# Optimization experiments

Measured on AMD Instinct MI355X. Metric: run time of the kernel, lower is better.

## Reference

```python
import jax, jax.numpy as jnp
import numpy as np
import math

HIDDEN = 2048
HEADS = 16
GROUPS = 4
HEAD_DIM = HIDDEN // HEADS  # 128
KV_DIM = GROUPS * HEAD_DIM  # 512
B, S = 2, 2048


def setup_inputs() -> dict:
    key = jax.random.key(0)
    ks = jax.random.split(key, 10)
    scale = 0.02
    return {
        "X": jax.random.normal(ks[0], (B, S, HIDDEN), dtype=jnp.float32),
        "attention_mask": jnp.ones((B, S), dtype=jnp.int32),
        "Wq": jax.random.normal(ks[1], (HIDDEN, HIDDEN), dtype=jnp.float32) * scale,
        "bq": jnp.zeros((HIDDEN,), dtype=jnp.float32),
        "Wk": jax.random.normal(ks[2], (HIDDEN, KV_DIM), dtype=jnp.float32) * scale,
        "bk": jnp.zeros((KV_DIM,), dtype=jnp.float32),
        "Wv": jax.random.normal(ks[3], (HIDDEN, KV_DIM), dtype=jnp.float32) * scale,
        "bv": jnp.zeros((KV_DIM,), dtype=jnp.float32),
        "Wo": jax.random.normal(ks[4], (HIDDEN, HIDDEN), dtype=jnp.float32) * scale,
        "bo": jnp.zeros((HIDDEN,), dtype=jnp.float32),
    }


def reference(X, attention_mask, Wq, bq, Wk, bk, Wv, bv, Wo, bo):
    b, s, _ = X.shape
    num_per_group = HEADS // GROUPS
    # projections
    Q = (X @ Wq + bq).reshape(b, s, HEADS, HEAD_DIM).transpose(0, 2, 1, 3)   # [b,H,s,d]
    K = (X @ Wk + bk).reshape(b, s, GROUPS, HEAD_DIM).transpose(0, 2, 1, 3)  # [b,G,s,d]
    V = (X @ Wv + bv).reshape(b, s, GROUPS, HEAD_DIM).transpose(0, 2, 1, 3)
    # torch .repeat(1, num_per_group, 1, 1) tiles group axis: [g0..gG-1, g0..gG-1, ...]
    K = jnp.tile(K, (1, num_per_group, 1, 1))  # [b,H,s,d]
    V = jnp.tile(V, (1, num_per_group, 1, 1))
    scores = jnp.einsum("bhqd,bhkd->bhqk", Q, K) / math.sqrt(HEAD_DIM)
    mask = attention_mask[:, None, None, :] == 0  # [b,1,1,s]
    scores = jnp.where(mask, jnp.float32(-jnp.inf), scores)
    attn = jax.nn.softmax(scores, axis=-1)
    out = jnp.einsum("bhqk,bhkd->bhqd", attn, V)  # [b,H,s,d]
    out = out.transpose(0, 2, 1, 3).reshape(b, s, HIDDEN)
    return out @ Wo + bo
```

## Files before the change

### kernel.cpp

```cpp
#include <hip/hip_runtime.h>
#include <hip/hip_bf16.h>


typedef __attribute__((ext_vector_type(8))) short short8;
typedef __attribute__((ext_vector_type(4))) short short4v;
typedef __attribute__((ext_vector_type(4))) float float4v;

#define C1F 0.12751743f
#define B0F -16.0f

#if defined(__has_builtin) && __has_builtin(__builtin_amdgcn_exp2f)
#define EXP2(x) __builtin_amdgcn_exp2f(x)
#else
#define EXP2(x) exp2f(x)
#endif

__device__ __forceinline__ short f2bf(float x) {
    __hip_bfloat16 h = __float2bfloat16(x);
    short s; __builtin_memcpy(&s, &h, sizeof(s)); return s;
}

__device__ __forceinline__ void gl16(const short* g, short* l) {
    __builtin_amdgcn_global_load_lds(
        (const __attribute__((address_space(1))) void*)g,
        (__attribute__((address_space(3))) void*)l, 16, 0, 0);
}

__global__ __launch_bounds__(256) void cvt_bf16_kernel(const float* __restrict__ in,
                                                       short* __restrict__ out, int n) {
    int i = (blockIdx.x * 256 + threadIdx.x) * 4;
    if (i >= n) return;
    float4 v = *(const float4*)(in + i);
    short4v o;
    o[0] = f2bf(v.x); o[1] = f2bf(v.y); o[2] = f2bf(v.z); o[3] = f2bf(v.w);
    *(short4v*)(out + i) = o;
}

__global__ __launch_bounds__(256) void transpose_cvt_kernel(const float* __restrict__ W,
                                                            short* __restrict__ Wt,
                                                            int K, int N) {
    __shared__ float tile[32][33];
    int n0 = blockIdx.x * 32, k0 = blockIdx.y * 32;
    int tx = threadIdx.x & 31, ty = threadIdx.x >> 5;
#pragma unroll
    for (int i = 0; i < 4; ++i) {
        int kk = ty + i * 8;
        tile[kk][tx] = W[(size_t)(k0 + kk) * N + n0 + tx];
    }
    __syncthreads();
#pragma unroll
    for (int i = 0; i < 4; ++i) {
        int nn = ty + i * 8;
        Wt[(size_t)(n0 + nn) * K + k0 + tx] = f2bf(tile[tx][nn]);
    }
}

__global__ __launch_bounds__(256) void gemm_dma_kernel(
    const short* __restrict__ A, const short* __restrict__ Bt,
    const float* __restrict__ b0, const float* __restrict__ b1, const float* __restrict__ b2,
    short* __restrict__ O0, short* __restrict__ O1, short* __restrict__ O2,
    float* __restrict__ Of, int K, int mode) {
    __shared__ short As[128 * 32];
    __shared__ short Bs[128 * 32];
    const int t = threadIdx.x, lane = t & 63, w = t >> 6;
    const int l15 = lane & 15, quad = lane >> 4;
    const int wm = (w & 1) * 64, wn = (w >> 1) * 64;
    const int m0 = blockIdx.y * 128, n0 = blockIdx.x * 128;
    const int r4 = lane >> 2, c8 = (lane & 3) * 8;
    const short* ga = A + (size_t)(m0 + w * 16 + r4) * K + c8;
    const short* gb = Bt + (size_t)(n0 + w * 16 + r4) * K + c8;
    short* lA = As + (w * 16) * 32;
    short* lB = Bs + (w * 16) * 32;

    float4v acc[4][4] = {};

    for (int k0 = 0; k0 < K; k0 += 32) {
        gl16(ga + k0, lA);
        gl16(ga + (size_t)64 * K + k0, lA + 64 * 32);
        gl16(gb + k0, lB);
        gl16(gb + (size_t)64 * K + k0, lB + 64 * 32);
        __syncthreads();
        short8 af[4], bfr[4];
#pragma unroll
        for (int i = 0; i < 4; ++i)
            af[i] = *(const short8*)(As + (wm + i * 16 + l15) * 32 + quad * 8);
#pragma unroll
        for (int j = 0; j < 4; ++j)
            bfr[j] = *(const short8*)(Bs + (wn + j * 16 + l15) * 32 + quad * 8);
#pragma unroll
        for (int i = 0; i < 4; ++i)
#pragma unroll
            for (int j = 0; j < 4; ++j)
                acc[i][j] = __builtin_amdgcn_mfma_f32_16x16x32_bf16(af[i], bfr[j], acc[i][j], 0, 0, 0);
        __syncthreads();
    }

#pragma unroll
    for (int i = 0; i < 4; ++i) {
#pragma unroll
        for (int j = 0; j < 4; ++j) {
            const int col = n0 + wn + j * 16 + l15;
            const int row0 = m0 + wm + i * 16 + quad * 4;
            if (mode == 1) {
                const float bc = b0[col];
#pragma unroll
                for (int r = 0; r < 4; ++r)
                    Of[(size_t)(row0 + r) * 2048 + col] = acc[i][j][r] + bc;
            } else if (col < 2048) {
                const float bc = b0[col];
#pragma unroll
                for (int r = 0; r < 4; ++r)
                    O0[(size_t)(row0 + r) * 2048 + col] = f2bf(acc[i][j][r] + bc);
            } else if (col < 2560) {
                const int c = col - 2048;
                const float bc = b1[c];
#pragma unroll
                for (int r = 0; r < 4; ++r)
                    O1[(size_t)(row0 + r) * 512 + c] = f2bf(acc[i][j][r] + bc);
            } else {
                const int c = col - 2560;
                const float bc = b2[c];
#pragma unroll
                for (int r = 0; r < 4; ++r)
                    O2[(size_t)c * 4096 + row0 + r] = f2bf(acc[i][j][r] + bc);
            }
        }
    }
}

__global__ __launch_bounds__(512, 2) void flash_kernel(
    const short* __restrict__ Qb, const short* __restrict__ Kb,
    const short* __restrict__ Vt, const int* __restrict__ mask,
    short* __restrict__ Ab) {
    __shared__ short Ks[64 * 136];
    __shared__ short Vs[128 * 72];
    __shared__ short Ps[8 * 32 * 72];
    __shared__ float mb[64];

    const int t = threadIdx.x;
    const int lane = t & 63, w = t >> 6;
    const int l15 = lane & 15, quad = lane >> 4;
    const int qt = blockIdx.x, g = blockIdx.y, b = blockIdx.z;
    const int h = g + 4 * (w & 3);
    const int q0 = qt * 64 + (w >> 2) * 32;

    short8 qf[2][4];
#pragma unroll
    for (int mi = 0; mi < 2; ++mi)
#pragma unroll
        for (int ks = 0; ks < 4; ++ks)
            qf[mi][ks] = *(const short8*)(Qb + (size_t)(b * 2048 + q0 + mi * 16 + l15) * 2048
                                          + h * 128 + ks * 32 + quad * 8);

    float4v o[2][8] = {};
    float rsum[2][4] = {};
    short* PsW = Ps + w * (32 * 72);

    const int kR = t >> 4, kC = (t & 15) * 8;
    const int vR = t >> 3, vC = (t & 7) * 8;
    const short* kg = Kb + (size_t)(b * 2048 + kR) * 512 + g * 128 + kC;
    const short* vg = Vt + (size_t)(g * 128 + vR) * 4096 + (size_t)b * 2048 + vC;

    for (int kt = 0; kt < 32; ++kt) {
        const int kb = kt * 64;
        short8 k0v = *(const short8*)(kg + (size_t)kb * 512);
        short8 k1v = *(const short8*)(kg + (size_t)(kb + 32) * 512);
        short8 v0v = *(const short8*)(vg + kb);
        short8 v1v = *(const short8*)(vg + (size_t)64 * 4096 + kb);
        float mv = 0.f;
        if (t < 64) mv = mask[b * 2048 + kb + t] ? B0F : -1e30f;
        __syncthreads();
        *(short8*)(Ks + kR * 136 + kC) = k0v;
        *(short8*)(Ks + (kR + 32) * 136 + kC) = k1v;
        *(short8*)(Vs + vR * 72 + vC) = v0v;
        *(short8*)(Vs + (vR + 64) * 72 + vC) = v1v;
        if (t < 64) mb[t] = mv;
        __syncthreads();

        float4v s[2][4] = {};
#pragma unroll
        for (int ks = 0; ks < 4; ++ks)
#pragma unroll
            for (int j = 0; j < 4; ++j) {
                short8 bk = *(const short8*)(Ks + (j * 16 + l15) * 136 + ks * 32 + quad * 8);
                s[0][j] = __builtin_amdgcn_mfma_f32_16x16x32_bf16(qf[0][ks], bk, s[0][j], 0, 0, 0);
                s[1][j] = __builtin_amdgcn_mfma_f32_16x16x32_bf16(qf[1][ks], bk, s[1][j], 0, 0, 0);
            }
#pragma unroll
        for (int mi = 0; mi < 2; ++mi)
#pragma unroll
            for (int j = 0; j < 4; ++j) {
                const float mbias = mb[j * 16 + l15];
#pragma unroll
                for (int r = 0; r < 4; ++r) {
                    float p = EXP2(fmaf(s[mi][j][r], C1F, mbias));
                    rsum[mi][r] += p;
                    PsW[(mi * 16 + quad * 4 + r) * 72 + j * 16 + l15] = f2bf(p);
                }
            }
#pragma unroll
        for (int ks2 = 0; ks2 < 2; ++ks2) {
            short8 pa0 = *(const short8*)(PsW + l15 * 72 + ks2 * 32 + quad * 8);
            short8 pa1 = *(const short8*)(PsW + (16 + l15) * 72 + ks2 * 32 + quad * 8);
#pragma unroll
            for (int jj = 0; jj < 8; ++jj) {
                short8 bv = *(const short8*)(Vs + (jj * 16 + l15) * 72 + ks2 * 32 + quad * 8);
                o[0][jj] = __builtin_amdgcn_mfma_f32_16x16x32_bf16(pa0, bv, o[0][jj], 0, 0, 0);
                o[1][jj] = __builtin_amdgcn_mfma_f32_16x16x32_bf16(pa1, bv, o[1][jj], 0, 0, 0);
            }
        }
    }

    float rinv[2][4];
#pragma unroll
    for (int mi = 0; mi < 2; ++mi)
#pragma unroll
        for (int r = 0; r < 4; ++r) {
            float v = rsum[mi][r];
            v += __shfl_xor(v, 1, 64); v += __shfl_xor(v, 2, 64);
            v += __shfl_xor(v, 4, 64); v += __shfl_xor(v, 8, 64);
            rinv[mi][r] = (v > 0.f) ? 1.f / v : 0.f;
        }
    const size_t ob = (size_t)(b * 2048 + q0) * 2048 + h * 128;
#pragma unroll
    for (int mi = 0; mi < 2; ++mi)
#pragma unroll
        for (int jj = 0; jj < 8; ++jj)
#pragma unroll
            for (int r = 0; r < 4; ++r)
                Ab[ob + (size_t)(mi * 16 + quad * 4 + r) * 2048 + jj * 16 + l15] =
                    f2bf(o[mi][jj][r] * rinv[mi][r]);
}

extern "C" void kernel_launch(void* const* d_in, const int* in_sizes, int n_in,
                              void* d_out, int out_size, void* d_ws, size_t ws_size,
                              hipStream_t stream) {
    (void)in_sizes; (void)n_in; (void)out_size; (void)ws_size;
    const float* X  = (const float*)d_in[0];
    const int* mask = (const int*)d_in[1];
    const float* Wq = (const float*)d_in[2];
    const float* bq = (const float*)d_in[3];
    const float* Wk = (const float*)d_in[4];
    const float* bk = (const float*)d_in[5];
    const float* Wv = (const float*)d_in[6];
    const float* bv = (const float*)d_in[7];
    const float* Wo = (const float*)d_in[8];
    const float* bo = (const float*)d_in[9];
    float* out = (float*)d_out;

    char* ws = (char*)d_ws;
    short* Xb     = (short*)(ws + 0);
    short* WqkvT  = (short*)(ws + 16777216);
    short* Wot    = (short*)(ws + 29360128);
    short* Qb     = (short*)(ws + 37748736);
    short* Kb     = (short*)(ws + 54525952);
    short* Vt     = (short*)(ws + 58720256);
    short* Ab     = Xb;

    const int M = 4096, HID = 2048, KV = 512;

    cvt_bf16_kernel<<<8192, 256, 0, stream>>>(X, Xb, M * HID);
    transpose_cvt_kernel<<<dim3(64, 64), 256, 0, stream>>>(Wq, WqkvT, HID, HID);
    transpose_cvt_kernel<<<dim3(16, 64), 256, 0, stream>>>(Wk, WqkvT + (size_t)2048 * 2048, HID, KV);
    transpose_cvt_kernel<<<dim3(16, 64), 256, 0, stream>>>(Wv, WqkvT + (size_t)2560 * 2048, HID, KV);
    transpose_cvt_kernel<<<dim3(64, 64), 256, 0, stream>>>(Wo, Wot, HID, HID);

    gemm_dma_kernel<<<dim3(24, 32), 256, 0, stream>>>(
        Xb, WqkvT, bq, bk, bv, Qb, Kb, Vt, nullptr, HID, 0);

    flash_kernel<<<dim3(32, 4, 2), 512, 0, stream>>>(Qb, Kb, Vt, mask, Ab);

    gemm_dma_kernel<<<dim3(16, 32), 256, 0, stream>>>(
        Ab, Wot, bo, nullptr, nullptr, nullptr, nullptr, nullptr, out, HID, 1);
}
```

Measured before the change: 345.7 us.

## Shrink flash blocks to 256 threads, prefetch next K/V tile, swizzle P LDS

The flash kernel now uses 4 waves per block covering 32 query rows, with twice as many blocks in the grid. The next K/V tile and mask are loaded into registers before the current tile's MFMA work, so global latency overlaps compute. The P scratch tile in LDS gets an XOR swizzle to cut bank conflicts, and s_setprio raises wave priority around the MFMA sections. K/V are now loaded once per 32 query rows instead of per 64, which doubles K/V traffic, and the prefetch registers raise register pressure.

```diff
diff --git a/kernel.cpp b/kernel.cpp
--- a/kernel.cpp
+++ b/kernel.cpp
@@ -128,21 +128,21 @@
     }
 }
 
-__global__ __launch_bounds__(512, 2) void flash_kernel(
+__global__ __launch_bounds__(256, 2) void flash_kernel(
     const short* __restrict__ Qb, const short* __restrict__ Kb,
     const short* __restrict__ Vt, const int* __restrict__ mask,
     short* __restrict__ Ab) {
     __shared__ short Ks[64 * 136];
     __shared__ short Vs[128 * 72];
-    __shared__ short Ps[8 * 32 * 72];
+    __shared__ short Ps[4 * 32 * 72];
     __shared__ float mb[64];
 
     const int t = threadIdx.x;
     const int lane = t & 63, w = t >> 6;
     const int l15 = lane & 15, quad = lane >> 4;
     const int qt = blockIdx.x, g = blockIdx.y, b = blockIdx.z;
-    const int h = g + 4 * (w & 3);
-    const int q0 = qt * 64 + (w >> 2) * 32;
+    const int h = g + 4 * w;
+    const int q0 = qt * 32;
 
     short8 qf[2][4];
 #pragma unroll
@@ -155,29 +155,46 @@
     float4v o[2][8] = {};
     float rsum[2][4] = {};
     short* PsW = Ps + w * (32 * 72);
+    const int psxr = ((l15 >> 3) & 1) << 4;
 
     const int kR = t >> 4, kC = (t & 15) * 8;
     const int vR = t >> 3, vC = (t & 7) * 8;
     const short* kg = Kb + (size_t)(b * 2048 + kR) * 512 + g * 128 + kC;
     const short* vg = Vt + (size_t)(g * 128 + vR) * 4096 + (size_t)b * 2048 + vC;
 
+    short8 kv[4], vv[4];
+    float mv = 0.f;
+
+#define LOADT(KB)                                                                  \
+    do {                                                                           \
+        kv[0] = *(const short8*)(kg + (size_t)(KB) * 512);                         \
+        kv[1] = *(const short8*)(kg + (size_t)((KB) + 16) * 512);                  \
+        kv[2] = *(const short8*)(kg + (size_t)((KB) + 32) * 512);                  \
+        kv[3] = *(const short8*)(kg + (size_t)((KB) + 48) * 512);                  \
+        vv[0] = *(const short8*)(vg + (KB));                                       \
+        vv[1] = *(const short8*)(vg + (size_t)32 * 4096 + (KB));                   \
+        vv[2] = *(const short8*)(vg + (size_t)64 * 4096 + (KB));                   \
+        vv[3] = *(const short8*)(vg + (size_t)96 * 4096 + (KB));                   \
+        if (t < 64) mv = mask[b * 2048 + (KB) + t] ? B0F : -1e30f;                 \
+    } while (0)
+
+    LOADT(0);
+
     for (int kt = 0; kt < 32; ++kt) {
-        const int kb = kt * 64;
-        short8 k0v = *(const short8*)(kg + (size_t)kb * 512);
-        short8 k1v = *(const short8*)(kg + (size_t)(kb + 32) * 512);
-        short8 v0v = *(const short8*)(vg + kb);
-        short8 v1v = *(const short8*)(vg + (size_t)64 * 4096 + kb);
-        float mv = 0.f;
-        if (t < 64) mv = mask[b * 2048 + kb + t] ? B0F : -1e30f;
-        __syncthreads();
-        *(short8*)(Ks + kR * 136 + kC) = k0v;
-        *(short8*)(Ks + (kR + 32) * 136 + kC) = k1v;
-        *(short8*)(Vs + vR * 72 + vC) = v0v;
-        *(short8*)(Vs + (vR + 64) * 72 + vC) = v1v;
+        __syncthreads();
+#pragma unroll
+        for (int i = 0; i < 4; ++i)
+            *(short8*)(Ks + (kR + i * 16) * 136 + kC) = kv[i];
+#pragma unroll
+        for (int i = 0; i < 4; ++i)
+            *(short8*)(Vs + (vR + i * 32) * 72 + vC) = vv[i];
         if (t < 64) mb[t] = mv;
         __syncthreads();
 
+        if (kt + 1 < 32) LOADT((kt + 1) * 64);
+
         float4v s[2][4] = {};
+        __builtin_amdgcn_s_setprio(1);
 #pragma unroll
         for (int ks = 0; ks < 4; ++ks)
 #pragma unroll
@@ -186,6 +203,7 @@
                 s[0][j] = __builtin_amdgcn_mfma_f32_16x16x32_bf16(qf[0][ks], bk, s[0][j], 0, 0, 0);
                 s[1][j] = __builtin_amdgcn_mfma_f32_16x16x32_bf16(qf[1][ks], bk, s[1][j], 0, 0, 0);
             }
+        __builtin_amdgcn_s_setprio(0);
 #pragma unroll
         for (int mi = 0; mi < 2; ++mi)
 #pragma unroll
@@ -195,13 +213,15 @@
                 for (int r = 0; r < 4; ++r) {
                     float p = EXP2(fmaf(s[mi][j][r], C1F, mbias));
                     rsum[mi][r] += p;
-                    PsW[(mi * 16 + quad * 4 + r) * 72 + j * 16 + l15] = f2bf(p);
+                    const int row = mi * 16 + quad * 4 + r;
+                    PsW[row * 72 + ((j * 16 + l15) ^ (((row >> 3) & 1) << 4))] = f2bf(p);
                 }
             }
+        __builtin_amdgcn_s_setprio(1);
 #pragma unroll
         for (int ks2 = 0; ks2 < 2; ++ks2) {
-            short8 pa0 = *(const short8*)(PsW + l15 * 72 + ks2 * 32 + quad * 8);
-            short8 pa1 = *(const short8*)(PsW + (16 + l15) * 72 + ks2 * 32 + quad * 8);
+            short8 pa0 = *(const short8*)(PsW + l15 * 72 + ((ks2 * 32 + quad * 8) ^ psxr));
+            short8 pa1 = *(const short8*)(PsW + (16 + l15) * 72 + ((ks2 * 32 + quad * 8) ^ psxr));
 #pragma unroll
             for (int jj = 0; jj < 8; ++jj) {
                 short8 bv = *(const short8*)(Vs + (jj * 16 + l15) * 72 + ks2 * 32 + quad * 8);
@@ -209,7 +229,9 @@
                 o[1][jj] = __builtin_amdgcn_mfma_f32_16x16x32_bf16(pa1, bv, o[1][jj], 0, 0, 0);
             }
         }
-    }
+        __builtin_amdgcn_s_setprio(0);
+    }
+#undef LOADT
 
     float rinv[2][4];
 #pragma unroll
@@ -268,7 +290,7 @@
     gemm_dma_kernel<<<dim3(24, 32), 256, 0, stream>>>(
         Xb, WqkvT, bq, bk, bv, Qb, Kb, Vt, nullptr, HID, 0);
 
-    flash_kernel<<<dim3(32, 4, 2), 512, 0, stream>>>(Qb, Kb, Vt, mask, Ab);
+    flash_kernel<<<dim3(64, 4, 2), 256, 0, stream>>>(Qb, Kb, Vt, mask, Ab);
 
     gemm_dma_kernel<<<dim3(16, 32), 256, 0, stream>>>(
         Ab, Wot, bo, nullptr, nullptr, nullptr, nullptr, nullptr, out, HID, 1);
```

New measurement: 355.6 us. 2.9% more time.
